# Kernel optimization log

Measured on AMD Instinct MI355X. Metric: run time of the kernel, lower is better.

## Reference

```python
import jax, jax.numpy as jnp
import numpy as np


def _gcn_conv(x, edge_index_sl, deg_inv_sqrt, W, b, num_nodes):
    """One GCNConv layer (PyG semantics, normalize=True, self-loops already in edge_index_sl)."""
    h = x @ W  # [N, F_out] dense projection first (F_out <= F_in)
    src = edge_index_sl[0]
    dst = edge_index_sl[1]
    norm = deg_inv_sqrt[src] * deg_inv_sqrt[dst]  # [E+N]
    msg = h[src] * norm[:, None]                  # gather + scale
    out = jax.ops.segment_sum(msg, dst, num_segments=num_nodes)  # scatter-add
    return out + b


def _prep_graph(edge_index, num_nodes):
    # GCNConv(normalize=True) adds self-loops, then deg over destination nodes.
    loops = jnp.arange(num_nodes, dtype=edge_index.dtype)
    ei = jnp.concatenate([edge_index, jnp.stack([loops, loops])], axis=1)  # [2, E+N]
    deg = jax.ops.segment_sum(jnp.ones(ei.shape[1], dtype=jnp.float32), ei[1], num_segments=num_nodes)
    deg_inv_sqrt = jnp.where(deg > 0, jax.lax.rsqrt(deg), 0.0)
    return ei, deg_inv_sqrt


def setup_inputs() -> dict:
    key = jax.random.key(0)
    k1, k2, k3, k4 = jax.random.split(key, 4)
    N, E, D_IN, D_H, D_OUT = 100000, 1200000, 128, 64, 1
    x = jax.random.normal(k1, (N, D_IN), dtype=jnp.float32)
    edge_index = jax.random.randint(k2, (2, E), 0, N, dtype=jnp.int64)
    # Glorot-ish init for weights
    W1 = jax.random.normal(k3, (D_IN, D_H), dtype=jnp.float32) * (1.0 / np.sqrt(D_IN))
    b1 = jnp.zeros((D_H,), dtype=jnp.float32)
    W2 = jax.random.normal(k4, (D_H, D_OUT), dtype=jnp.float32) * (1.0 / np.sqrt(D_H))
    b2 = jnp.zeros((D_OUT,), dtype=jnp.float32)
    return {"x": x, "edge_index": edge_index, "W1": W1, "b1": b1, "W2": W2, "b2": b2}


def reference(x, edge_index, W1, b1, W2, b2):
    num_nodes = x.shape[0]
    ei, dinv = _prep_graph(edge_index, num_nodes)
    h = jax.nn.relu(_gcn_conv(x, ei, dinv, W1, b1, num_nodes))
    # F.dropout(training=self.training) is identity in eval mode (reference baseline)
    out = _gcn_conv(h, ei, dinv, W2, b2, num_nodes)
    return out
```

## Files before the change

kernel.cpp:

```cpp
#include <hip/hip_runtime.h>


#define NBLK 256
#define MAXB 8192

__device__ __forceinline__ float bf2f(unsigned short u) {
    union { unsigned int i; float f; } v; v.i = ((unsigned int)u) << 16; return v.f;
}
__device__ __forceinline__ unsigned short f2bf(float f) {
    union { float f; unsigned int i; } v; v.f = f;
    unsigned int r = (v.i + 0x7fffu + ((v.i >> 16) & 1u)) >> 16;
    return (unsigned short)r;
}

__global__ __launch_bounds__(256) void k_hist(const int* __restrict__ dst, int E, int chunk,
                                              int NB, int* __restrict__ bh) {
    __shared__ int h[512];
    int blk = blockIdx.x, t = threadIdx.x;
    h[t] = 0; h[t + 256] = 0;
    __syncthreads();
    int e0 = blk * chunk, e1 = min(E, e0 + chunk);
    for (int e = e0 + t; e < e1; e += 256) atomicAdd(&h[dst[e] >> 8], 1);
    __syncthreads();
    for (int k = t; k < NB; k += 256) bh[blk * NB + k] = h[k];
}

__global__ __launch_bounds__(256) void k_bscan(int* __restrict__ bh, int NB,
                                               int* __restrict__ btot) {
    __shared__ int s[256];
    int k = blockIdx.x, t = threadIdx.x;
    int v = bh[t * NB + k];
    s[t] = v;
    __syncthreads();
    for (int off = 1; off < 256; off <<= 1) {
        int u = (t >= off) ? s[t - off] : 0;
        __syncthreads();
        s[t] += u;
        __syncthreads();
    }
    bh[t * NB + k] = s[t] - v;
    if (t == 255) btot[k] = s[255];
}

__global__ __launch_bounds__(512) void k_cscan(const int* __restrict__ btot, int NB, int E,
                                               int* __restrict__ bbase, int* __restrict__ offs,
                                               int N) {
    __shared__ int s[512];
    int t = threadIdx.x;
    int v = (t < NB) ? btot[t] : 0;
    s[t] = v;
    __syncthreads();
    for (int off = 1; off < 512; off <<= 1) {
        int u = (t >= off) ? s[t - off] : 0;
        __syncthreads();
        s[t] += u;
        __syncthreads();
    }
    if (t < NB) bbase[t] = s[t] - v;
    if (t == 0) offs[N] = E;
}

__global__ __launch_bounds__(256) void k_dscatter(const int* __restrict__ src,
                                                  const int* __restrict__ dst, int E, int chunk,
                                                  const int* __restrict__ bh,
                                                  const int* __restrict__ bbase, int NB,
                                                  unsigned int* __restrict__ grouped) {
    __shared__ int cur[512];
    int blk = blockIdx.x, t = threadIdx.x;
    for (int k = t; k < NB; k += 256) cur[k] = bbase[k] + bh[blk * NB + k];
    __syncthreads();
    int e0 = blk * chunk, e1 = min(E, e0 + chunk);
    for (int e = e0 + t; e < e1; e += 256) {
        int d = dst[e];
        int pos = atomicAdd(&cur[d >> 8], 1);
        grouped[pos] = ((unsigned int)src[e] << 8) | (unsigned int)(d & 255);
    }
}

__global__ __launch_bounds__(256) void k_bfill(const unsigned int* __restrict__ grouped,
                                               const int* __restrict__ bbase,
                                               const int* __restrict__ btot, int N,
                                               int* __restrict__ offs, int* __restrict__ csr,
                                               float* __restrict__ dinv) {
    __shared__ int hist[256], pfx[256], cur[256];
    __shared__ int stage[MAXB];
    int k = blockIdx.x, t = threadIdx.x;
    int base = bbase[k], cnt = btot[k];
    hist[t] = 0;
    __syncthreads();
    for (int i = t; i < cnt; i += 256) atomicAdd(&hist[grouped[base + i] & 255u], 1);
    __syncthreads();
    int v = hist[t];
    pfx[t] = v;
    __syncthreads();
    for (int off = 1; off < 256; off <<= 1) {
        int u = (t >= off) ? pfx[t - off] : 0;
        __syncthreads();
        pfx[t] += u;
        __syncthreads();
    }
    int excl = pfx[t] - v;
    cur[t] = excl;
    int node = (k << 8) + t;
    if (node < N) {
        offs[node] = base + excl;
        dinv[node] = rsqrtf((float)v + 1.0f);
    }
    __syncthreads();
    if (cnt <= MAXB) {
        for (int i = t; i < cnt; i += 256) {
            unsigned int p = grouped[base + i];
            int pos = atomicAdd(&cur[p & 255u], 1);
            stage[pos] = (int)(p >> 8);
        }
        __syncthreads();
        for (int i = t; i < cnt; i += 256) csr[base + i] = stage[i];
    } else {
        for (int i = t; i < cnt; i += 256) {
            unsigned int p = grouped[base + i];
            int pos = atomicAdd(&cur[p & 255u], 1);
            csr[base + pos] = (int)(p >> 8);
        }
    }
}

__global__ __launch_bounds__(256) void k_gemm1(
    const float* __restrict__ x, const float* __restrict__ W1,
    const float* __restrict__ dinv, unsigned short* __restrict__ ppb, int N)
{
    __shared__ float xs[64][132];
    __shared__ float ws[128][64];
    int tid = threadIdx.x;
    int row0 = blockIdx.x * 64;
    {
        const float4* w4 = (const float4*)W1;
        float4* s4 = (float4*)&ws[0][0];
        #pragma unroll
        for (int i = 0; i < 8; i++) s4[tid + 256 * i] = w4[tid + 256 * i];
    }
    {
        int maxr = N - row0; if (maxr > 64) maxr = 64;
        const float4* x4 = (const float4*)(x + (size_t)row0 * 128);
        int n4 = maxr * 32;
        for (int i = tid; i < n4; i += 256) {
            int r = i >> 5, c = i & 31;
            *(float4*)&xs[r][c * 4] = x4[i];
        }
    }
    __syncthreads();
    int c0 = (tid & 15) * 4;
    int r0 = (tid >> 4) * 4;
    float acc[4][4] = {};
    for (int kk = 0; kk < 128; kk += 4) {
        float xv[4][4], wv[4][4];
        #pragma unroll
        for (int i = 0; i < 4; i++) *(float4*)xv[i] = *(const float4*)&xs[r0 + i][kk];
        #pragma unroll
        for (int t = 0; t < 4; t++) *(float4*)wv[t] = *(const float4*)&ws[kk + t][c0];
        #pragma unroll
        for (int i = 0; i < 4; i++)
            #pragma unroll
            for (int j = 0; j < 4; j++)
                acc[i][j] += xv[i][0] * wv[0][j] + xv[i][1] * wv[1][j]
                           + xv[i][2] * wv[2][j] + xv[i][3] * wv[3][j];
    }
    #pragma unroll
    for (int i = 0; i < 4; i++) {
        int r = row0 + r0 + i;
        if (r < N) {
            float d = dinv[r];
            ushort4 o;
            o.x = f2bf(acc[i][0] * d);
            o.y = f2bf(acc[i][1] * d);
            o.z = f2bf(acc[i][2] * d);
            o.w = f2bf(acc[i][3] * d);
            *(ushort4*)&ppb[(size_t)r * 64 + c0] = o;
        }
    }
}

__global__ void k_fused1(const int* __restrict__ offs, const int* __restrict__ csr,
                         const unsigned short* __restrict__ ppb,
                         const float* __restrict__ dinv, const float* __restrict__ b1,
                         const float* __restrict__ W2, float* __restrict__ qp, int N) {
    int t = blockIdx.x * blockDim.x + threadIdx.x;
    int lane = t & 63;
    int half = lane >> 5;
    int hl = lane & 31;
    int node = t >> 6;
    int nstride = (gridDim.x * blockDim.x) >> 6;
    float w2a = W2[2 * hl], w2b = W2[2 * hl + 1];
    float ba = b1[2 * hl], bb = b1[2 * hl + 1];
    for (; node < N; node += nstride) {
        int start = offs[node], end = offs[node + 1];
        float acca = 0.0f, accb = 0.0f;
        if (half == 0) {
            unsigned int v = *(const unsigned int*)&ppb[(size_t)node * 64 + 2 * hl];
            acca = bf2f((unsigned short)v);
            accb = bf2f((unsigned short)(v >> 16));
        }
        for (int j0 = start; j0 < end; j0 += 64) {
            int jj = j0 + lane;
            int idx = (jj < end) ? csr[jj] : 0;
            int cnt = end - j0; if (cnt > 64) cnt = 64;
            for (int kk = 0; kk < cnt; kk += 2) {
                int s0 = __shfl(idx, kk, 64);
                int s1 = (kk + 1 < cnt) ? __shfl(idx, kk + 1, 64) : -1;
                int s = half ? s1 : s0;
                if (s >= 0) {
                    unsigned int v = *(const unsigned int*)&ppb[(size_t)s * 64 + 2 * hl];
                    acca += bf2f((unsigned short)v);
                    accb += bf2f((unsigned short)(v >> 16));
                }
            }
        }
        acca += __shfl_xor(acca, 32, 64);
        accb += __shfl_xor(accb, 32, 64);
        float di = dinv[node];
        float ha = fmaxf(di * acca + ba, 0.0f);
        float hb = fmaxf(di * accb + bb, 0.0f);
        float v = ha * w2a + hb * w2b;
        #pragma unroll
        for (int m = 16; m > 0; m >>= 1) v += __shfl_xor(v, m, 64);
        if (lane == 0) qp[node] = v * di;
    }
}

__global__ void k_fused2(const int* __restrict__ offs, const int* __restrict__ csr,
                         const float* __restrict__ qp, const float* __restrict__ dinv,
                         const float* __restrict__ b2, float* __restrict__ out, int N) {
    int i = blockIdx.x * blockDim.x + threadIdx.x;
    if (i < N) {
        int start = offs[i], end = offs[i + 1];
        float s = qp[i];
        for (int j = start; j < end; j++) s += qp[csr[j]];
        out[i] = dinv[i] * s + b2[0];
    }
}

extern "C" void kernel_launch(void* const* d_in, const int* in_sizes, int n_in,
                              void* d_out, int out_size, void* d_ws, size_t ws_size,
                              hipStream_t stream) {
    const float* x  = (const float*)d_in[0];
    const int*   ei = (const int*)d_in[1];
    const float* W1 = (const float*)d_in[2];
    const float* b1 = (const float*)d_in[3];
    const float* W2 = (const float*)d_in[4];
    const float* b2 = (const float*)d_in[5];
    float* out = (float*)d_out;

    int N = in_sizes[0] / 128;
    int E = in_sizes[1] / 2;
    const int* src = ei;
    const int* dst = ei + E;
    int NB = (N + 255) >> 8;
    int chunk = (E + NBLK - 1) / NBLK;

    size_t Np = ((size_t)N + 255) & ~(size_t)255;
    size_t Ep = ((size_t)E + 255) & ~(size_t)255;
    char* w = (char*)d_ws;
    int* bh      = (int*)w;            w += (size_t)NBLK * 512 * 4;
    int* btot    = (int*)w;            w += 512 * 4;
    int* bbase   = (int*)w;            w += 512 * 4;
    unsigned int* grouped = (unsigned int*)w;  w += Ep * 4;
    int* offs    = (int*)w;            w += (Np + 256) * 4;
    int* csr     = (int*)w;            w += Ep * 4;
    float* dinv  = (float*)w;          w += Np * 4;
    unsigned short* ppb = (unsigned short*)w;  w += Np * 64 * 2;
    float* qp    = (float*)w;

    k_hist<<<NBLK, 256, 0, stream>>>(dst, E, chunk, NB, bh);
    k_bscan<<<NB, 256, 0, stream>>>(bh, NB, btot);
    k_cscan<<<1, 512, 0, stream>>>(btot, NB, E, bbase, offs, N);
    k_dscatter<<<NBLK, 256, 0, stream>>>(src, dst, E, chunk, bh, bbase, NB, grouped);
    k_bfill<<<NB, 256, 0, stream>>>(grouped, bbase, btot, N, offs, csr, dinv);
    k_gemm1<<<(N + 63) / 64, 256, 0, stream>>>(x, W1, dinv, ppb, N);
    k_fused1<<<2048, 256, 0, stream>>>(offs, csr, ppb, dinv, b1, W2, qp, N);
    k_fused2<<<(N + 255) / 256, 256, 0, stream>>>(offs, csr, qp, dinv, b2, out, N);
}
```

Before: 226.5 us.

## Replace CSR build with bucket-grouped shared-memory atomic aggregation

Removes the per-node CSR construction (offsets and sorted column array) and computes degrees in a lighter kernel. Both aggregation layers now process each 256-node destination bucket in one block, accumulating gathered features into shared memory with atomic adds, with column rotation to spread bank accesses. This saves the CSR fill pass and its memory traffic, but adds many LDS float atomics and uses a large shared-memory footprint that limits occupancy.

```diff
diff --git a/kernel.cpp b/kernel.cpp
--- a/kernel.cpp
+++ b/kernel.cpp
@@ -2,7 +2,6 @@
 
 
 #define NBLK 256
-#define MAXB 8192
 
 __device__ __forceinline__ float bf2f(unsigned short u) {
     union { unsigned int i; float f; } v; v.i = ((unsigned int)u) << 16; return v.f;
@@ -42,9 +41,8 @@
     if (t == 255) btot[k] = s[255];
 }
 
-__global__ __launch_bounds__(512) void k_cscan(const int* __restrict__ btot, int NB, int E,
-                                               int* __restrict__ bbase, int* __restrict__ offs,
-                                               int N) {
+__global__ __launch_bounds__(512) void k_cscan(const int* __restrict__ btot, int NB,
+                                               int* __restrict__ bbase) {
     __shared__ int s[512];
     int t = threadIdx.x;
     int v = (t < NB) ? btot[t] : 0;
@@ -57,7 +55,6 @@
         __syncthreads();
     }
     if (t < NB) bbase[t] = s[t] - v;
-    if (t == 0) offs[N] = E;
 }
 
 __global__ __launch_bounds__(256) void k_dscatter(const int* __restrict__ src,
@@ -77,51 +74,19 @@
     }
 }
 
-__global__ __launch_bounds__(256) void k_bfill(const unsigned int* __restrict__ grouped,
-                                               const int* __restrict__ bbase,
-                                               const int* __restrict__ btot, int N,
-                                               int* __restrict__ offs, int* __restrict__ csr,
-                                               float* __restrict__ dinv) {
-    __shared__ int hist[256], pfx[256], cur[256];
-    __shared__ int stage[MAXB];
-    int k = blockIdx.x, t = threadIdx.x;
+__global__ __launch_bounds__(256) void k_degdinv(const unsigned int* __restrict__ grouped,
+                                                 const int* __restrict__ bbase,
+                                                 const int* __restrict__ btot, int N,
+                                                 float* __restrict__ dinv) {
+    __shared__ int h[256];
+    int k = blockIdx.x, t = threadIdx.x;
+    h[t] = 0;
+    __syncthreads();
     int base = bbase[k], cnt = btot[k];
-    hist[t] = 0;
-    __syncthreads();
-    for (int i = t; i < cnt; i += 256) atomicAdd(&hist[grouped[base + i] & 255u], 1);
-    __syncthreads();
-    int v = hist[t];
-    pfx[t] = v;
-    __syncthreads();
-    for (int off = 1; off < 256; off <<= 1) {
-        int u = (t >= off) ? pfx[t - off] : 0;
-        __syncthreads();
-        pfx[t] += u;
-        __syncthreads();
-    }
-    int excl = pfx[t] - v;
-    cur[t] = excl;
+    for (int i = t; i < cnt; i += 256) atomicAdd(&h[grouped[base + i] & 255u], 1);
+    __syncthreads();
     int node = (k << 8) + t;
-    if (node < N) {
-        offs[node] = base + excl;
-        dinv[node] = rsqrtf((float)v + 1.0f);
-    }
-    __syncthreads();
-    if (cnt <= MAXB) {
-        for (int i = t; i < cnt; i += 256) {
-            unsigned int p = grouped[base + i];
-            int pos = atomicAdd(&cur[p & 255u], 1);
-            stage[pos] = (int)(p >> 8);
-        }
-        __syncthreads();
-        for (int i = t; i < cnt; i += 256) csr[base + i] = stage[i];
-    } else {
-        for (int i = t; i < cnt; i += 256) {
-            unsigned int p = grouped[base + i];
-            int pos = atomicAdd(&cur[p & 255u], 1);
-            csr[base + pos] = (int)(p >> 8);
-        }
-    }
+    if (node < N) dinv[node] = rsqrtf((float)h[t] + 1.0f);
 }
 
 __global__ __launch_bounds__(256) void k_gemm1(
@@ -179,63 +144,84 @@
     }
 }
 
-__global__ void k_fused1(const int* __restrict__ offs, const int* __restrict__ csr,
-                         const unsigned short* __restrict__ ppb,
-                         const float* __restrict__ dinv, const float* __restrict__ b1,
-                         const float* __restrict__ W2, float* __restrict__ qp, int N) {
-    int t = blockIdx.x * blockDim.x + threadIdx.x;
-    int lane = t & 63;
-    int half = lane >> 5;
-    int hl = lane & 31;
-    int node = t >> 6;
-    int nstride = (gridDim.x * blockDim.x) >> 6;
-    float w2a = W2[2 * hl], w2b = W2[2 * hl + 1];
-    float ba = b1[2 * hl], bb = b1[2 * hl + 1];
-    for (; node < N; node += nstride) {
-        int start = offs[node], end = offs[node + 1];
-        float acca = 0.0f, accb = 0.0f;
-        if (half == 0) {
-            unsigned int v = *(const unsigned int*)&ppb[(size_t)node * 64 + 2 * hl];
-            acca = bf2f((unsigned short)v);
-            accb = bf2f((unsigned short)(v >> 16));
-        }
-        for (int j0 = start; j0 < end; j0 += 64) {
-            int jj = j0 + lane;
-            int idx = (jj < end) ? csr[jj] : 0;
-            int cnt = end - j0; if (cnt > 64) cnt = 64;
-            for (int kk = 0; kk < cnt; kk += 2) {
-                int s0 = __shfl(idx, kk, 64);
-                int s1 = (kk + 1 < cnt) ? __shfl(idx, kk + 1, 64) : -1;
-                int s = half ? s1 : s0;
-                if (s >= 0) {
-                    unsigned int v = *(const unsigned int*)&ppb[(size_t)s * 64 + 2 * hl];
-                    acca += bf2f((unsigned short)v);
-                    accb += bf2f((unsigned short)(v >> 16));
-                }
+__global__ __launch_bounds__(1024) void k_fused1(const unsigned int* __restrict__ grouped,
+                                                 const int* __restrict__ bbase,
+                                                 const int* __restrict__ btot,
+                                                 const unsigned short* __restrict__ ppb,
+                                                 const float* __restrict__ dinv,
+                                                 const float* __restrict__ b1,
+                                                 const float* __restrict__ W2,
+                                                 float* __restrict__ qp, int N) {
+    __shared__ float acc[256 * 64];
+    int k = blockIdx.x, t = threadIdx.x;
+    {
+        float4 z = make_float4(0.f, 0.f, 0.f, 0.f);
+        float4* a4 = (float4*)acc;
+        #pragma unroll
+        for (int i = 0; i < 4; i++) a4[t + 1024 * i] = z;
+    }
+    __syncthreads();
+    int base = bbase[k], cnt = btot[k];
+    int lane = t & 63, wid = t >> 6;
+    int hl = lane & 31, half = lane >> 5;
+    for (int i0 = wid * 64; i0 < cnt; i0 += 16 * 64) {
+        int m = cnt - i0; if (m > 64) m = 64;
+        unsigned int idx = (lane < m) ? grouped[base + i0 + lane] : 0u;
+        for (int kk = 0; kk < m; kk += 2) {
+            int kk1 = (kk + 1 < m) ? kk + 1 : kk;
+            unsigned int p0 = __shfl(idx, kk, 64);
+            unsigned int p1 = __shfl(idx, kk1, 64);
+            unsigned int p = half ? p1 : p0;
+            bool act = (!half) || (kk + 1 < m);
+            if (act) {
+                int s = (int)(p >> 8);
+                int d = (int)(p & 255u);
+                unsigned int v = *(const unsigned int*)&ppb[(size_t)s * 64 + 2 * hl];
+                float f0 = bf2f((unsigned short)(v & 0xffffu));
+                float f1 = bf2f((unsigned short)(v >> 16));
+                int c0 = (2 * hl + d) & 63;
+                int c1 = (2 * hl + 1 + d) & 63;
+                atomicAdd(&acc[d * 64 + c0], f0);
+                atomicAdd(&acc[d * 64 + c1], f1);
             }
         }
-        acca += __shfl_xor(acca, 32, 64);
-        accb += __shfl_xor(accb, 32, 64);
+    }
+    __syncthreads();
+    float w2 = W2[lane];
+    float bb = b1[lane];
+    for (int d = wid * 16; d < wid * 16 + 16; d++) {
+        int node = (k << 8) + d;
+        if (node >= N) break;
+        float a = acc[d * 64 + ((lane + d) & 63)];
+        a += bf2f(ppb[(size_t)node * 64 + lane]);
         float di = dinv[node];
-        float ha = fmaxf(di * acca + ba, 0.0f);
-        float hb = fmaxf(di * accb + bb, 0.0f);
-        float v = ha * w2a + hb * w2b;
-        #pragma unroll
-        for (int m = 16; m > 0; m >>= 1) v += __shfl_xor(v, m, 64);
+        float h = fmaxf(di * a + bb, 0.0f);
+        float v = h * w2;
+        #pragma unroll
+        for (int m = 32; m > 0; m >>= 1) v += __shfl_xor(v, m, 64);
         if (lane == 0) qp[node] = v * di;
     }
 }
 
-__global__ void k_fused2(const int* __restrict__ offs, const int* __restrict__ csr,
-                         const float* __restrict__ qp, const float* __restrict__ dinv,
-                         const float* __restrict__ b2, float* __restrict__ out, int N) {
-    int i = blockIdx.x * blockDim.x + threadIdx.x;
-    if (i < N) {
-        int start = offs[i], end = offs[i + 1];
-        float s = qp[i];
-        for (int j = start; j < end; j++) s += qp[csr[j]];
-        out[i] = dinv[i] * s + b2[0];
-    }
+__global__ __launch_bounds__(256) void k_fused2(const unsigned int* __restrict__ grouped,
+                                                const int* __restrict__ bbase,
+                                                const int* __restrict__ btot,
+                                                const float* __restrict__ qp,
+                                                const float* __restrict__ dinv,
+                                                const float* __restrict__ b2,
+                                                float* __restrict__ out, int N) {
+    __shared__ float a2[256];
+    int k = blockIdx.x, t = threadIdx.x;
+    a2[t] = 0.0f;
+    __syncthreads();
+    int base = bbase[k], cnt = btot[k];
+    for (int i = t; i < cnt; i += 256) {
+        unsigned int p = grouped[base + i];
+        atomicAdd(&a2[p & 255u], qp[p >> 8]);
+    }
+    __syncthreads();
+    int node = (k << 8) + t;
+    if (node < N) out[node] = dinv[node] * (a2[t] + qp[node]) + b2[0];
 }
 
 extern "C" void kernel_launch(void* const* d_in, const int* in_sizes, int n_in,
@@ -263,18 +249,16 @@
     int* btot    = (int*)w;            w += 512 * 4;
     int* bbase   = (int*)w;            w += 512 * 4;
     unsigned int* grouped = (unsigned int*)w;  w += Ep * 4;
-    int* offs    = (int*)w;            w += (Np + 256) * 4;
-    int* csr     = (int*)w;            w += Ep * 4;
     float* dinv  = (float*)w;          w += Np * 4;
     unsigned short* ppb = (unsigned short*)w;  w += Np * 64 * 2;
     float* qp    = (float*)w;
 
     k_hist<<<NBLK, 256, 0, stream>>>(dst, E, chunk, NB, bh);
     k_bscan<<<NB, 256, 0, stream>>>(bh, NB, btot);
-    k_cscan<<<1, 512, 0, stream>>>(btot, NB, E, bbase, offs, N);
+    k_cscan<<<1, 512, 0, stream>>>(btot, NB, bbase);
     k_dscatter<<<NBLK, 256, 0, stream>>>(src, dst, E, chunk, bh, bbase, NB, grouped);
-    k_bfill<<<NB, 256, 0, stream>>>(grouped, bbase, btot, N, offs, csr, dinv);
+    k_degdinv<<<NB, 256, 0, stream>>>(grouped, bbase, btot, N, dinv);
     k_gemm1<<<(N + 63) / 64, 256, 0, stream>>>(x, W1, dinv, ppb, N);
-    k_fused1<<<2048, 256, 0, stream>>>(offs, csr, ppb, dinv, b1, W2, qp, N);
-    k_fused2<<<(N + 255) / 256, 256, 0, stream>>>(offs, csr, qp, dinv, b2, out, N);
-}
+    k_fused1<<<NB, 1024, 0, stream>>>(grouped, bbase, btot, ppb, dinv, b1, W2, qp, N);
+    k_fused2<<<NB, 256, 0, stream>>>(grouped, bbase, btot, qp, dinv, b2, out, N);
+}
```

Result: slower. 714.4 us (+215.5%).
